# Performance work log

Measured on AMD Instinct MI355X. Metric: run time of the kernel, lower is better.

## Reference

```python
import jax, jax.numpy as jnp
import numpy as np

N, M, D, K = 32768, 1024, 512, 4096  # frames, motion_dim, latent_dim, codebook size
COMMITMENT_COST = 0.25
BN_EPS = 1e-5


def setup_inputs() -> dict:
    key = jax.random.key(0)
    ks = jax.random.split(key, 4)
    return {
        "x": jax.random.normal(ks[0], (N, M), dtype=jnp.float32),
        "enc_w": jax.random.normal(ks[1], (D, M), dtype=jnp.float32) * (1.0 / np.sqrt(M)),
        "enc_b": jnp.zeros((D,), jnp.float32),
        "bn_gamma": jnp.ones((D,), jnp.float32),
        "bn_beta": jnp.zeros((D,), jnp.float32),
        "bn_mean": jnp.zeros((D,), jnp.float32),
        "bn_var": jnp.ones((D,), jnp.float32),
        # nn.Embedding init: uniform(-1/K, 1/K)
        "codebook": jax.random.uniform(ks[2], (K, D), dtype=jnp.float32, minval=-1.0 / K, maxval=1.0 / K),
        "dec_w": jax.random.normal(ks[3], (M, D), dtype=jnp.float32) * (1.0 / np.sqrt(D)),
        "dec_b": jnp.zeros((M,), jnp.float32),
    }


def reference(x, enc_w, enc_b, bn_gamma, bn_beta, bn_mean, bn_var, codebook, dec_w, dec_b):
    # Encoder linear: [N, M] -> [N, D]
    z = x @ enc_w.T + enc_b
    # BatchNorm1d (inference mode, running stats)
    z = (z - bn_mean) * jax.lax.rsqrt(bn_var + BN_EPS) * bn_gamma + bn_beta

    # VQ (VQ_Payam_EMA, eval): squared L2 distances via ||z||^2 + ||e||^2 - 2 z e^T
    # distances: [N, K]
    distances = (
        jnp.sum(z * z, axis=1, keepdims=True)
        + jnp.sum(codebook * codebook, axis=1)
        - 2.0 * (z @ codebook.T)
    )
    idx = jnp.argmin(distances, axis=1)                    # [N]
    encodings = jax.nn.one_hot(idx, K, dtype=z.dtype)      # [N, K] one-hot scatter
    quantized = codebook[idx]                              # gather == encodings @ codebook

    # commitment loss (EMA variant: only e_latent_loss, quantized detached)
    e_latent_loss = jnp.mean((jax.lax.stop_gradient(quantized) - z) ** 2)
    loss = COMMITMENT_COST * e_latent_loss

    # straight-through estimator
    quantized_st = z + jax.lax.stop_gradient(quantized - z)

    avg_probs = jnp.mean(encodings, axis=0)                # [K]
    perplexity = jnp.exp(-jnp.sum(avg_probs * jnp.log(avg_probs + 1e-10)))

    # Decoder linear: [N, D] -> [N, M]
    out = quantized_st @ dec_w.T + dec_b
    return out, loss, perplexity, encodings
```

## Files before the change

### kernel.cpp

```cpp
#include <hip/hip_runtime.h>
#include <math.h>
#include <float.h>

#define N_FR 32768
#define M_DIM 1024
#define D_DIM 512
#define K_CB 4096

static const long long OUT_ELEMS = (long long)N_FR * M_DIM;
static const long long LOSS_OFF  = OUT_ELEMS;
static const long long ENC_OFF   = OUT_ELEMS + 2;
static const long long Z_OFF   = ENC_OFF + 2;
static const long long DC_OFF  = Z_OFF  + (long long)N_FR * D_DIM;
static const long long XH_OFF  = DC_OFF + (long long)K_CB * M_DIM;
static const long long XL_OFF  = XH_OFF + (long long)N_FR * M_DIM / 2;
static const long long WH_OFF  = XL_OFF + (long long)N_FR * M_DIM / 2;
static const long long WL_OFF  = WH_OFF + (long long)D_DIM * M_DIM / 2;
static const long long CH_OFF  = WL_OFF + (long long)D_DIM * M_DIM / 2;
static const long long CL_OFF  = CH_OFF + (long long)K_CB * D_DIM / 2;
static const long long ZH_OFF  = CL_OFF + (long long)K_CB * D_DIM / 2;
static const long long ZL_OFF  = ZH_OFF + (long long)N_FR * D_DIM / 2;
static const long long PV_OFF  = ZL_OFF + (long long)N_FR * D_DIM / 2;
static const long long PI_OFF  = PV_OFF + 4LL * N_FR;
static const long long DWH_OFF = PI_OFF + 4LL * N_FR;
static const long long DWL_OFF = DWH_OFF + (long long)M_DIM * D_DIM / 2;
static const long long SNP_OFF = DWL_OFF + (long long)M_DIM * D_DIM / 2;
static const long long LP_OFF  = SNP_OFF + 16LL * N_FR;

typedef __attribute__((ext_vector_type(8))) short bf16x8;
typedef __attribute__((ext_vector_type(8))) unsigned short u16x8;
typedef __attribute__((ext_vector_type(4))) float f32x4;

__device__ __forceinline__ unsigned short f2bf(float f) {
    unsigned u = __float_as_uint(f);
    return (unsigned short)((u + 0x7fffu + ((u >> 16) & 1u)) >> 16);
}
__device__ __forceinline__ float bf2f(unsigned short h) {
    return __uint_as_float(((unsigned)h) << 16);
}
__device__ __forceinline__ void gl_lds16(const unsigned short* g, unsigned short* l) {
    __builtin_amdgcn_global_load_lds(
        (const __attribute__((address_space(1))) unsigned int*)g,
        (__attribute__((address_space(3))) unsigned int*)l,
        16, 0, 0);
}

__device__ __forceinline__ void conv_body(const float* in, unsigned short* hi,
                                          unsigned short* lo, int C, int KC, int w)
{
    int lane = threadIdx.x & 63;
    int bn = w / KC, ck = w % KC;
    int r = bn * 16 + (lane & 15);
    int c = ck * 32 + (lane >> 4) * 8;
    const float4* p = (const float4*)&in[(size_t)r * C + c];
    float4 v0 = p[0], v1 = p[1];
    float f[8] = {v0.x, v0.y, v0.z, v0.w, v1.x, v1.y, v1.z, v1.w};
    u16x8 hv, lv;
    #pragma unroll
    for (int j = 0; j < 8; ++j) {
        unsigned short h = f2bf(f[j]);
        hv[j] = h;
        lv[j] = f2bf(f[j] - bf2f(h));
    }
    size_t o = (size_t)w * 512 + lane * 8;
    *(u16x8*)&hi[o] = hv;
    *(u16x8*)&lo[o] = lv;
}

__global__ __launch_bounds__(256)
void conv_all(const float* __restrict__ x,  const float* __restrict__ ew,
              const float* __restrict__ cb, const float* __restrict__ dw,
              unsigned short* __restrict__ xh,  unsigned short* __restrict__ xl,
              unsigned short* __restrict__ wh,  unsigned short* __restrict__ wl,
              unsigned short* __restrict__ ch,  unsigned short* __restrict__ cl,
              unsigned short* __restrict__ dwh, unsigned short* __restrict__ dwl)
{
    int b = blockIdx.x;
    const float* in; unsigned short* hi; unsigned short* lo; int C; int w0;
    if (b < 16384)      { in = x;  hi = xh;  lo = xl;  C = 1024; w0 = b; }
    else if (b < 16640) { in = ew; hi = wh;  lo = wl;  C = 1024; w0 = b - 16384; }
    else if (b < 17664) { in = cb; hi = ch;  lo = cl;  C = 512;  w0 = b - 16640; }
    else                { in = dw; hi = dwh; lo = dwl; C = 512;  w0 = b - 17664; }
    int KC = C / 32;
    conv_body(in, hi, lo, C, KC, w0 * 4 + (threadIdx.x >> 6));
}

__global__ __launch_bounds__(256)
void conv_z(const float* __restrict__ z, unsigned short* __restrict__ zh,
            unsigned short* __restrict__ zl, float* __restrict__ snp)
{
    int w = blockIdx.x * 4 + (threadIdx.x >> 6);
    int lane = threadIdx.x & 63;
    int bn = w >> 4, ck = w & 15;
    int r = bn * 16 + (lane & 15);
    int c = ck * 32 + (lane >> 4) * 8;
    const float4* p = (const float4*)&z[(size_t)r * D_DIM + c];
    float4 v0 = p[0], v1 = p[1];
    float f[8] = {v0.x, v0.y, v0.z, v0.w, v1.x, v1.y, v1.z, v1.w};
    u16x8 hv, lv;
    float s = 0.f;
    #pragma unroll
    for (int j = 0; j < 8; ++j) {
        unsigned short h = f2bf(f[j]);
        hv[j] = h;
        lv[j] = f2bf(f[j] - bf2f(h));
        s = fmaf(f[j], f[j], s);
    }
    size_t o = (size_t)w * 512 + lane * 8;
    *(u16x8*)&zh[o] = hv;
    *(u16x8*)&zl[o] = lv;
    s += __shfl_xor(s, 16);
    s += __shfl_xor(s, 32);
    if ((lane >> 4) == 0) snp[(size_t)ck * N_FR + r] = s;
}

template<int EPI>
__global__ __launch_bounds__(256, 2)
void gemm_pack(const unsigned short* __restrict__ ah_, const unsigned short* __restrict__ al_,
               const unsigned short* __restrict__ bh_, const unsigned short* __restrict__ bl_,
               const float* __restrict__ bias, const float* __restrict__ gamma,
               const float* __restrict__ beta, const float* __restrict__ mean,
               const float* __restrict__ var, float* __restrict__ C,
               int nbi, int nkb, int NJ)
{
    __shared__ unsigned short lds[32768];
    const int tid = threadIdx.x, wid = tid >> 6, lane = tid & 63;
    const int wr = wid >> 1, wc = wid & 1;
    const int bi = blockIdx.x % nbi, bj = blockIdx.x / nbi;

    auto stage = [&](int ks, int bufsel) {
        unsigned short* dst = lds + bufsel * 16384;
        #pragma unroll
        for (int q = 0; q < 8; ++q) {
            int id = wid * 8 + q;
            int arr = id >> 3, rb = id & 7;
            const unsigned short* base = arr == 0 ? ah_ : arr == 1 ? al_ : arr == 2 ? bh_ : bl_;
            size_t b = (size_t)((arr < 2 ? bi : bj) * 8 + rb) * nkb + ks;
            gl_lds16(base + b * 512 + lane * 8, dst + id * 512);
        }
    };

    f32x4 acc[4][4];
    #pragma unroll
    for (int i = 0; i < 4; ++i)
        #pragma unroll
        for (int j = 0; j < 4; ++j) acc[i][j] = (f32x4){0.f, 0.f, 0.f, 0.f};

    stage(0, 0);
    __syncthreads();

    for (int ks = 0; ks < nkb; ++ks) {
        int cur = ks & 1;
        if (ks + 1 < nkb) stage(ks + 1, cur ^ 1);
        const unsigned short* L = lds + cur * 16384;
        bf16x8 ah[4], al[4], bh[4], bl[4];
        #pragma unroll
        for (int i = 0; i < 4; ++i) {
            ah[i] = *(const bf16x8*)(L + (4 * wr + i) * 512 + lane * 8);
            al[i] = *(const bf16x8*)(L + 4096 + (4 * wr + i) * 512 + lane * 8);
        }
        #pragma unroll
        for (int j = 0; j < 4; ++j) {
            bh[j] = *(const bf16x8*)(L + 8192  + (4 * wc + j) * 512 + lane * 8);
            bl[j] = *(const bf16x8*)(L + 12288 + (4 * wc + j) * 512 + lane * 8);
        }
        #pragma unroll
        for (int i = 0; i < 4; ++i)
            #pragma unroll
            for (int j = 0; j < 4; ++j) {
                acc[i][j] = __builtin_amdgcn_mfma_f32_16x16x32_bf16(ah[i], bh[j], acc[i][j], 0, 0, 0);
                acc[i][j] = __builtin_amdgcn_mfma_f32_16x16x32_bf16(ah[i], bl[j], acc[i][j], 0, 0, 0);
                acc[i][j] = __builtin_amdgcn_mfma_f32_16x16x32_bf16(al[i], bh[j], acc[i][j], 0, 0, 0);
            }
        __syncthreads();
    }
    #pragma unroll
    for (int j = 0; j < 4; ++j) {
        int col = bj * 128 + wc * 64 + j * 16 + (lane & 15);
        float bvv = bias[col];
        float g = 0.f, bt = 0.f, mn = 0.f, rs = 0.f;
        if (EPI == 0) {
            g  = gamma[col];
            bt = beta[col];
            mn = mean[col];
            rs = (float)(1.0 / sqrt((double)var[col] + 1e-5));
        }
        #pragma unroll
        for (int i = 0; i < 4; ++i)
            #pragma unroll
            for (int r = 0; r < 4; ++r) {
                int row = bi * 128 + wr * 64 + i * 16 + (lane >> 4) * 4 + r;
                float v = acc[i][j][r] + bvv;
                if (EPI == 0) v = (v - mn) * rs * g + bt;
                C[(size_t)row * NJ + col] = v;
            }
    }
}

__global__ __launch_bounds__(256, 2)
void argmin_mfma(const unsigned short* __restrict__ zh, const unsigned short* __restrict__ zl,
                 const unsigned short* __restrict__ ch,
                 const float* __restrict__ se,
                 float* __restrict__ pval, int* __restrict__ pidx)
{
    __shared__ unsigned short lds[32768];
    __shared__ float sv[128][2];
    __shared__ int   si[128][2];
    const int tid = threadIdx.x, wid = tid >> 6, lane = tid & 63;
    const int wr = wid >> 1, wc = wid & 1;
    const int row0 = (int)(blockIdx.x & 255) * 128;
    const int grp  = (int)(blockIdx.x >> 8);

    auto stage = [&](int t, int bufsel) {
        int cc = t >> 4, ks = t & 15;
        int code0 = grp * 1024 + cc * 256;
        unsigned short* dst = lds + bufsel * 16384;
        #pragma unroll
        for (int q = 0; q < 8; ++q) {
            int id = wid * 8 + q;
            const unsigned short* src;
            if (id < 16) {
                int a = id >> 3, rb = id & 7;
                src = (a ? zl : zh) + ((size_t)((row0 >> 4) + rb) * 16 + ks) * 512 + lane * 8;
            } else {
                int cb2 = id - 16;
                src = ch + ((size_t)((code0 >> 4) + cb2) * 16 + ks) * 512 + lane * 8;
            }
            gl_lds16(src, dst + id * 512);
        }
    };

    float bv[16];
    int   bi[16];
    #pragma unroll
    for (int s = 0; s < 16; ++s) { bv[s] = FLT_MAX; bi[s] = 0x7fffffff; }

    f32x4 acc[4][8];
    #pragma unroll
    for (int i = 0; i < 4; ++i)
        #pragma unroll
        for (int j = 0; j < 8; ++j) acc[i][j] = (f32x4){0.f, 0.f, 0.f, 0.f};

    stage(0, 0);
    __syncthreads();

    for (int t = 0; t < 64; ++t) {
        int cur = t & 1;
        if (t < 63) stage(t + 1, cur ^ 1);
        const unsigned short* L = lds + cur * 16384;
        bf16x8 ah[4], al[4];
        #pragma unroll
        for (int i = 0; i < 4; ++i) {
            ah[i] = *(const bf16x8*)(L + (wr * 4 + i) * 512 + lane * 8);
            al[i] = *(const bf16x8*)(L + 4096 + (wr * 4 + i) * 512 + lane * 8);
        }
        #pragma unroll
        for (int j = 0; j < 8; ++j) {
            bf16x8 bhj = *(const bf16x8*)(L + 8192 + (wc * 8 + j) * 512 + lane * 8);
            #pragma unroll
            for (int i = 0; i < 4; ++i) {
                acc[i][j] = __builtin_amdgcn_mfma_f32_16x16x32_bf16(ah[i], bhj, acc[i][j], 0, 0, 0);
                acc[i][j] = __builtin_amdgcn_mfma_f32_16x16x32_bf16(al[i], bhj, acc[i][j], 0, 0, 0);
            }
        }
        if ((t & 15) == 15) {
            int code0 = grp * 1024 + (t >> 4) * 256;
            #pragma unroll
            for (int j = 0; j < 8; ++j) {
                int code = code0 + wc * 128 + j * 16 + (lane & 15);
                float sev = se[code];
                #pragma unroll
                for (int i = 0; i < 4; ++i)
                    #pragma unroll
                    for (int r = 0; r < 4; ++r) {
                        float key = sev - 2.0f * acc[i][j][r];
                        int s = i * 4 + r;
                        if (key < bv[s]) { bv[s] = key; bi[s] = code; }
                        acc[i][j][r] = 0.f;
                    }
            }
        }
        __syncthreads();
    }

    #pragma unroll
    for (int s = 0; s < 16; ++s) {
        #pragma unroll
        for (int off = 1; off < 16; off <<= 1) {
            float ov = __shfl_xor(bv[s], off);
            int   oi = __shfl_xor(bi[s], off);
            if (ov < bv[s] || (ov == bv[s] && oi < bi[s])) { bv[s] = ov; bi[s] = oi; }
        }
    }
    if ((lane & 15) == 0) {
        #pragma unroll
        for (int i = 0; i < 4; ++i)
            #pragma unroll
            for (int r = 0; r < 4; ++r) {
                int row = wr * 64 + i * 16 + (lane >> 4) * 4 + r;
                sv[row][wc] = bv[i * 4 + r];
                si[row][wc] = bi[i * 4 + r];
            }
    }
    __syncthreads();
    if (tid < 128) {
        float v0 = sv[tid][0], v1 = sv[tid][1];
        int   i0 = si[tid][0], i1 = si[tid][1];
        float bvv = v0; int bii = i0;
        if (v1 < v0 || (v1 == v0 && i1 < i0)) { bvv = v1; bii = i1; }
        pval[(size_t)grp * N_FR + row0 + tid] = bvv;
        pidx[(size_t)grp * N_FR + row0 + tid] = bii;
    }
}

__global__ __launch_bounds__(256)
void merge_k(const float* __restrict__ pval, const int* __restrict__ pidx,
             const float* __restrict__ snp,
             int* __restrict__ fidx, int* __restrict__ counts,
             float* __restrict__ lpart)
{
    __shared__ float ls[4];
    int tid = threadIdx.x;
    int n = blockIdx.x * 256 + tid;
    float best = pval[n];
    int   bi   = pidx[n];
    #pragma unroll
    for (int c = 1; c < 4; ++c) {
        float v = pval[(long long)c * N_FR + n];
        int   i = pidx[(long long)c * N_FR + n];
        if (v < best) { best = v; bi = i; }
    }
    fidx[n] = bi;
    atomicAdd(&counts[bi], 1);
    float sn = 0.f;
    #pragma unroll
    for (int c = 0; c < 16; ++c) sn += snp[(long long)c * N_FR + n];
    float rl = sn + best;
    #pragma unroll
    for (int off = 32; off; off >>= 1) rl += __shfl_xor(rl, off);
    if ((tid & 63) == 0) ls[tid >> 6] = rl;
    __syncthreads();
    if (tid == 0) lpart[blockIdx.x] = ls[0] + ls[1] + ls[2] + ls[3];
}

__global__ __launch_bounds__(256)
void rownorm_k(const float* __restrict__ A, float* __restrict__ sn,
               int* __restrict__ counts)
{
    if (blockIdx.x < 16) counts[blockIdx.x * 256 + threadIdx.x] = 0;
    int row  = blockIdx.x * 4 + (threadIdx.x >> 6);
    int lane = threadIdx.x & 63;
    const float4* p = (const float4*)(A + (long long)row * D_DIM + lane * 8);
    float4 a = p[0], b = p[1];
    float s = a.x*a.x + a.y*a.y + a.z*a.z + a.w*a.w
            + b.x*b.x + b.y*b.y + b.z*b.z + b.w*b.w;
    #pragma unroll
    for (int off = 32; off; off >>= 1) s += __shfl_xor(s, off);
    if (lane == 0) sn[row] = s;
}

__global__ __launch_bounds__(256)
void gather_k(const float* __restrict__ DC, const int* __restrict__ fidx,
              float* __restrict__ outp)
{
    int n = blockIdx.x;
    int id = fidx[n];
    float4 v = ((const float4*)(DC + (long long)id * M_DIM))[threadIdx.x];
    ((float4*)(outp + (long long)n * M_DIM))[threadIdx.x] = v;
}

__global__ __launch_bounds__(256)
void enc_write(const int* __restrict__ fidx, float* __restrict__ enc)
{
    int n    = blockIdx.x * 4 + (threadIdx.x >> 6);
    int lane = threadIdx.x & 63;
    int idx  = fidx[n];
    f32x4* row = (f32x4*)(enc + (size_t)n * K_CB);
    #pragma unroll
    for (int c = 0; c < 16; ++c) {
        int p = c * 64 + lane;
        int b4 = p * 4;
        f32x4 v;
        v.x = (idx == b4 + 0) ? 1.0f : 0.0f;
        v.y = (idx == b4 + 1) ? 1.0f : 0.0f;
        v.z = (idx == b4 + 2) ? 1.0f : 0.0f;
        v.w = (idx == b4 + 3) ? 1.0f : 0.0f;
        __builtin_nontemporal_store(v, &row[p]);
    }
}

__global__ __launch_bounds__(256)
void fin_k(const int* __restrict__ counts, const float* __restrict__ lpart,
           float* __restrict__ scal)
{
    __shared__ double sh[4], lh[4];
    int tid = threadIdx.x;
    double s = 0.0;
    for (int k = tid; k < K_CB; k += 256) {
        double p = (double)counts[k] / (double)N_FR;
        s += p * log(p + 1e-10);
    }
    double l = (tid < 128) ? (double)lpart[tid] : 0.0;
    #pragma unroll
    for (int off = 32; off; off >>= 1) {
        s += __shfl_xor(s, off);
        l += __shfl_xor(l, off);
    }
    if ((tid & 63) == 0) { sh[tid >> 6] = s; lh[tid >> 6] = l; }
    __syncthreads();
    if (tid == 0) {
        double tot = sh[0] + sh[1] + sh[2] + sh[3];
        double L   = lh[0] + lh[1] + lh[2] + lh[3];
        scal[0] = (float)(0.25 * L / ((double)N_FR * (double)D_DIM));
        scal[1] = (float)exp(-tot);
    }
}

extern "C" void kernel_launch(void* const* d_in, const int* in_sizes, int n_in,
                              void* d_out, int out_size, void* d_ws, size_t ws_size,
                              hipStream_t stream)
{
    (void)in_sizes; (void)n_in; (void)out_size; (void)ws_size;
    const float* x        = (const float*)d_in[0];
    const float* enc_w    = (const float*)d_in[1];
    const float* enc_b    = (const float*)d_in[2];
    const float* bn_gamma = (const float*)d_in[3];
    const float* bn_beta  = (const float*)d_in[4];
    const float* bn_mean  = (const float*)d_in[5];
    const float* bn_var   = (const float*)d_in[6];
    const float* cb       = (const float*)d_in[7];
    const float* dec_w    = (const float*)d_in[8];
    const float* dec_b    = (const float*)d_in[9];

    float* outp = (float*)d_out;
    float* z    = outp + Z_OFF;
    float* dc   = outp + DC_OFF;
    unsigned short* xh  = (unsigned short*)(outp + XH_OFF);
    unsigned short* xl  = (unsigned short*)(outp + XL_OFF);
    unsigned short* whp = (unsigned short*)(outp + WH_OFF);
    unsigned short* wlp = (unsigned short*)(outp + WL_OFF);
    unsigned short* chp = (unsigned short*)(outp + CH_OFF);
    unsigned short* clp = (unsigned short*)(outp + CL_OFF);
    unsigned short* zhp = (unsigned short*)(outp + ZH_OFF);
    unsigned short* zlp = (unsigned short*)(outp + ZL_OFF);
    float* pval = outp + PV_OFF;
    int*   pidx = (int*)(outp + PI_OFF);
    unsigned short* dwh = (unsigned short*)(outp + DWH_OFF);
    unsigned short* dwl = (unsigned short*)(outp + DWL_OFF);
    float* snp   = outp + SNP_OFF;
    float* lpart = outp + LP_OFF;

    char*   wsb    = (char*)d_ws;
    int*    fidx   = (int*)wsb;
    int*    counts = (int*)(wsb + 131072);
    float*  se     = (float*)(wsb + 147456);

    conv_all<<<dim3(17920), 256, 0, stream>>>(x, enc_w, cb, dec_w,
        xh, xl, whp, wlp, chp, clp, dwh, dwl);
    rownorm_k<<<dim3(K_CB / 4), 256, 0, stream>>>(cb, se, counts);

    gemm_pack<0><<<dim3(1024), 256, 0, stream>>>(xh, xl, whp, wlp,
        enc_b, bn_gamma, bn_beta, bn_mean, bn_var, z, 256, 32, D_DIM);
    conv_z<<<dim3(8192), 256, 0, stream>>>(z, zhp, zlp, snp);

    gemm_pack<1><<<dim3(256), 256, 0, stream>>>(chp, clp, dwh, dwl,
        dec_b, nullptr, nullptr, nullptr, nullptr, dc, 32, 16, M_DIM);

    argmin_mfma<<<dim3(1024), 256, 0, stream>>>(zhp, zlp, chp, se, pval, pidx);
    merge_k<<<dim3(N_FR / 256), 256, 0, stream>>>(pval, pidx, snp, fidx, counts, lpart);

    gather_k<<<dim3(N_FR), 256, 0, stream>>>(dc, fidx, outp);
    fin_k<<<dim3(1), 256, 0, stream>>>(counts, lpart, outp + LOSS_OFF);

    enc_write<<<dim3(N_FR / 4), 256, 0, stream>>>(fidx, outp + ENC_OFF);
}
```

Measured before the change: 648.3 us.

## Switch GEMMs and argmin to 32x32x16 MFMA with repacked 32-row bf16 tiles

Repacks the hi/lo bf16 operand tiles into 32-row by 16-column blocks and replaces the 16x16x32 MFMA calls with 32x32x16 MFMA in the encoder, decoder and distance GEMMs. Larger MFMA tiles mean fewer LDS fragment loads per flop and fewer instructions issued. The argmin epilogue now reduces across lanes at every 256-code chunk and keeps running minima in shared memory instead of per-thread registers. This adds shuffle and LDS work per chunk, and the per-row norm partials double to 32 slices.

```diff
diff --git a/kernel.cpp b/kernel.cpp
--- a/kernel.cpp
+++ b/kernel.cpp
@@ -25,11 +25,12 @@
 static const long long DWH_OFF = PI_OFF + 4LL * N_FR;
 static const long long DWL_OFF = DWH_OFF + (long long)M_DIM * D_DIM / 2;
 static const long long SNP_OFF = DWL_OFF + (long long)M_DIM * D_DIM / 2;
-static const long long LP_OFF  = SNP_OFF + 16LL * N_FR;
-
-typedef __attribute__((ext_vector_type(8))) short bf16x8;
-typedef __attribute__((ext_vector_type(8))) unsigned short u16x8;
-typedef __attribute__((ext_vector_type(4))) float f32x4;
+static const long long LP_OFF  = SNP_OFF + 32LL * N_FR;
+
+typedef __attribute__((ext_vector_type(8)))  short bf16x8;
+typedef __attribute__((ext_vector_type(8)))  unsigned short u16x8;
+typedef __attribute__((ext_vector_type(4)))  float f32x4;
+typedef __attribute__((ext_vector_type(16))) float f32x16;
 
 __device__ __forceinline__ unsigned short f2bf(float f) {
     unsigned u = __float_as_uint(f);
@@ -44,14 +45,18 @@
         (__attribute__((address_space(3))) unsigned int*)l,
         16, 0, 0);
 }
+__device__ __forceinline__ f32x16 zero16() {
+    f32x16 z = {0.f,0.f,0.f,0.f,0.f,0.f,0.f,0.f,0.f,0.f,0.f,0.f,0.f,0.f,0.f,0.f};
+    return z;
+}
 
 __device__ __forceinline__ void conv_body(const float* in, unsigned short* hi,
-                                          unsigned short* lo, int C, int KC, int w)
+                                          unsigned short* lo, int C, int KC16, int w)
 {
     int lane = threadIdx.x & 63;
-    int bn = w / KC, ck = w % KC;
-    int r = bn * 16 + (lane & 15);
-    int c = ck * 32 + (lane >> 4) * 8;
+    int bn = w / KC16, ck = w % KC16;
+    int r = bn * 32 + (lane & 31);
+    int c = ck * 16 + (lane >> 5) * 8;
     const float4* p = (const float4*)&in[(size_t)r * C + c];
     float4 v0 = p[0], v1 = p[1];
     float f[8] = {v0.x, v0.y, v0.z, v0.w, v1.x, v1.y, v1.z, v1.w};
@@ -81,8 +86,8 @@
     else if (b < 16640) { in = ew; hi = wh;  lo = wl;  C = 1024; w0 = b - 16384; }
     else if (b < 17664) { in = cb; hi = ch;  lo = cl;  C = 512;  w0 = b - 16640; }
     else                { in = dw; hi = dwh; lo = dwl; C = 512;  w0 = b - 17664; }
-    int KC = C / 32;
-    conv_body(in, hi, lo, C, KC, w0 * 4 + (threadIdx.x >> 6));
+    int KC16 = C / 16;
+    conv_body(in, hi, lo, C, KC16, w0 * 4 + (threadIdx.x >> 6));
 }
 
 __global__ __launch_bounds__(256)
@@ -91,9 +96,9 @@
 {
     int w = blockIdx.x * 4 + (threadIdx.x >> 6);
     int lane = threadIdx.x & 63;
-    int bn = w >> 4, ck = w & 15;
-    int r = bn * 16 + (lane & 15);
-    int c = ck * 32 + (lane >> 4) * 8;
+    int bn = w >> 5, ck = w & 31;
+    int r = bn * 32 + (lane & 31);
+    int c = ck * 16 + (lane >> 5) * 8;
     const float4* p = (const float4*)&z[(size_t)r * D_DIM + c];
     float4 v0 = p[0], v1 = p[1];
     float f[8] = {v0.x, v0.y, v0.z, v0.w, v1.x, v1.y, v1.z, v1.w};
@@ -109,9 +114,8 @@
     size_t o = (size_t)w * 512 + lane * 8;
     *(u16x8*)&zh[o] = hv;
     *(u16x8*)&zl[o] = lv;
-    s += __shfl_xor(s, 16);
     s += __shfl_xor(s, 32);
-    if ((lane >> 4) == 0) snp[(size_t)ck * N_FR + r] = s;
+    if (lane < 32) snp[(size_t)ck * N_FR + r] = s;
 }
 
 template<int EPI>
@@ -121,7 +125,7 @@
                const float* __restrict__ bias, const float* __restrict__ gamma,
                const float* __restrict__ beta, const float* __restrict__ mean,
                const float* __restrict__ var, float* __restrict__ C,
-               int nbi, int nkb, int NJ)
+               int nbi, int nsteps, int nkb16, int NJ)
 {
     __shared__ unsigned short lds[32768];
     const int tid = threadIdx.x, wid = tid >> 6, lane = tid & 63;
@@ -133,50 +137,57 @@
         #pragma unroll
         for (int q = 0; q < 8; ++q) {
             int id = wid * 8 + q;
-            int arr = id >> 3, rb = id & 7;
+            int arr = id >> 3, idx = id & 7, rb = idx >> 1, kb = idx & 1;
             const unsigned short* base = arr == 0 ? ah_ : arr == 1 ? al_ : arr == 2 ? bh_ : bl_;
-            size_t b = (size_t)((arr < 2 ? bi : bj) * 8 + rb) * nkb + ks;
+            int bsel = (arr < 2) ? bi : bj;
+            size_t b = (size_t)(bsel * 4 + rb) * nkb16 + ks * 2 + kb;
             gl_lds16(base + b * 512 + lane * 8, dst + id * 512);
         }
     };
 
-    f32x4 acc[4][4];
-    #pragma unroll
-    for (int i = 0; i < 4; ++i)
-        #pragma unroll
-        for (int j = 0; j < 4; ++j) acc[i][j] = (f32x4){0.f, 0.f, 0.f, 0.f};
+    f32x16 acc[2][2];
+    #pragma unroll
+    for (int i = 0; i < 2; ++i)
+        #pragma unroll
+        for (int j = 0; j < 2; ++j) acc[i][j] = zero16();
 
     stage(0, 0);
     __syncthreads();
 
-    for (int ks = 0; ks < nkb; ++ks) {
+    for (int ks = 0; ks < nsteps; ++ks) {
         int cur = ks & 1;
-        if (ks + 1 < nkb) stage(ks + 1, cur ^ 1);
+        if (ks + 1 < nsteps) stage(ks + 1, cur ^ 1);
         const unsigned short* L = lds + cur * 16384;
-        bf16x8 ah[4], al[4], bh[4], bl[4];
-        #pragma unroll
-        for (int i = 0; i < 4; ++i) {
-            ah[i] = *(const bf16x8*)(L + (4 * wr + i) * 512 + lane * 8);
-            al[i] = *(const bf16x8*)(L + 4096 + (4 * wr + i) * 512 + lane * 8);
-        }
-        #pragma unroll
-        for (int j = 0; j < 4; ++j) {
-            bh[j] = *(const bf16x8*)(L + 8192  + (4 * wc + j) * 512 + lane * 8);
-            bl[j] = *(const bf16x8*)(L + 12288 + (4 * wc + j) * 512 + lane * 8);
-        }
-        #pragma unroll
-        for (int i = 0; i < 4; ++i)
-            #pragma unroll
-            for (int j = 0; j < 4; ++j) {
-                acc[i][j] = __builtin_amdgcn_mfma_f32_16x16x32_bf16(ah[i], bh[j], acc[i][j], 0, 0, 0);
-                acc[i][j] = __builtin_amdgcn_mfma_f32_16x16x32_bf16(ah[i], bl[j], acc[i][j], 0, 0, 0);
-                acc[i][j] = __builtin_amdgcn_mfma_f32_16x16x32_bf16(al[i], bh[j], acc[i][j], 0, 0, 0);
-            }
+        bf16x8 ah[2][2], al[2][2];
+        #pragma unroll
+        for (int i = 0; i < 2; ++i)
+            #pragma unroll
+            for (int kb = 0; kb < 2; ++kb) {
+                int blk = (wr * 2 + i) * 2 + kb;
+                ah[i][kb] = *(const bf16x8*)(L + blk * 512 + lane * 8);
+                al[i][kb] = *(const bf16x8*)(L + 4096 + blk * 512 + lane * 8);
+            }
+        #pragma unroll
+        for (int j = 0; j < 2; ++j) {
+            #pragma unroll
+            for (int kb = 0; kb < 2; ++kb) {
+                int blk = (wc * 2 + j) * 2 + kb;
+                bf16x8 bhj = *(const bf16x8*)(L + 8192  + blk * 512 + lane * 8);
+                bf16x8 blj = *(const bf16x8*)(L + 12288 + blk * 512 + lane * 8);
+                #pragma unroll
+                for (int i = 0; i < 2; ++i) {
+                    acc[i][j] = __builtin_amdgcn_mfma_f32_32x32x16_bf16(ah[i][kb], bhj, acc[i][j], 0, 0, 0);
+                    acc[i][j] = __builtin_amdgcn_mfma_f32_32x32x16_bf16(ah[i][kb], blj, acc[i][j], 0, 0, 0);
+                    acc[i][j] = __builtin_amdgcn_mfma_f32_32x32x16_bf16(al[i][kb], bhj, acc[i][j], 0, 0, 0);
+                }
+            }
+        }
         __syncthreads();
     }
-    #pragma unroll
-    for (int j = 0; j < 4; ++j) {
-        int col = bj * 128 + wc * 64 + j * 16 + (lane & 15);
+
+    #pragma unroll
+    for (int j = 0; j < 2; ++j) {
+        int col = bj * 128 + wc * 64 + j * 32 + (lane & 31);
         float bvv = bias[col];
         float g = 0.f, bt = 0.f, mn = 0.f, rs = 0.f;
         if (EPI == 0) {
@@ -186,11 +197,11 @@
             rs = (float)(1.0 / sqrt((double)var[col] + 1e-5));
         }
         #pragma unroll
-        for (int i = 0; i < 4; ++i)
-            #pragma unroll
-            for (int r = 0; r < 4; ++r) {
-                int row = bi * 128 + wr * 64 + i * 16 + (lane >> 4) * 4 + r;
-                float v = acc[i][j][r] + bvv;
+        for (int i = 0; i < 2; ++i)
+            #pragma unroll
+            for (int reg = 0; reg < 16; ++reg) {
+                int row = bi * 128 + wr * 64 + i * 32 + (reg & 3) + 8 * (reg >> 2) + 4 * (lane >> 5);
+                float v = acc[i][j][reg] + bvv;
                 if (EPI == 0) v = (v - mn) * rs * g + bt;
                 C[(size_t)row * NJ + col] = v;
             }
@@ -220,26 +231,25 @@
             int id = wid * 8 + q;
             const unsigned short* src;
             if (id < 16) {
-                int a = id >> 3, rb = id & 7;
-                src = (a ? zl : zh) + ((size_t)((row0 >> 4) + rb) * 16 + ks) * 512 + lane * 8;
+                int a = id >> 3, idx = id & 7, rb = idx >> 1, kb = idx & 1;
+                size_t b = (size_t)((row0 >> 5) + rb) * 32 + ks * 2 + kb;
+                src = (a ? zl : zh) + b * 512 + lane * 8;
             } else {
-                int cb2 = id - 16;
-                src = ch + ((size_t)((code0 >> 4) + cb2) * 16 + ks) * 512 + lane * 8;
+                int idx = id - 16, cb2 = idx >> 1, kb = idx & 1;
+                size_t b = (size_t)((code0 >> 5) + cb2) * 32 + ks * 2 + kb;
+                src = ch + b * 512 + lane * 8;
             }
             gl_lds16(src, dst + id * 512);
         }
     };
 
-    float bv[16];
-    int   bi[16];
-    #pragma unroll
-    for (int s = 0; s < 16; ++s) { bv[s] = FLT_MAX; bi[s] = 0x7fffffff; }
-
-    f32x4 acc[4][8];
-    #pragma unroll
-    for (int i = 0; i < 4; ++i)
-        #pragma unroll
-        for (int j = 0; j < 8; ++j) acc[i][j] = (f32x4){0.f, 0.f, 0.f, 0.f};
+    if (tid < 256) { sv[tid >> 1][tid & 1] = FLT_MAX; si[tid >> 1][tid & 1] = 0x7fffffff; }
+
+    f32x16 acc[2][4];
+    #pragma unroll
+    for (int i = 0; i < 2; ++i)
+        #pragma unroll
+        for (int j = 0; j < 4; ++j) acc[i][j] = zero16();
 
     stage(0, 0);
     __syncthreads();
@@ -248,61 +258,69 @@
         int cur = t & 1;
         if (t < 63) stage(t + 1, cur ^ 1);
         const unsigned short* L = lds + cur * 16384;
-        bf16x8 ah[4], al[4];
-        #pragma unroll
-        for (int i = 0; i < 4; ++i) {
-            ah[i] = *(const bf16x8*)(L + (wr * 4 + i) * 512 + lane * 8);
-            al[i] = *(const bf16x8*)(L + 4096 + (wr * 4 + i) * 512 + lane * 8);
-        }
-        #pragma unroll
-        for (int j = 0; j < 8; ++j) {
-            bf16x8 bhj = *(const bf16x8*)(L + 8192 + (wc * 8 + j) * 512 + lane * 8);
-            #pragma unroll
-            for (int i = 0; i < 4; ++i) {
-                acc[i][j] = __builtin_amdgcn_mfma_f32_16x16x32_bf16(ah[i], bhj, acc[i][j], 0, 0, 0);
-                acc[i][j] = __builtin_amdgcn_mfma_f32_16x16x32_bf16(al[i], bhj, acc[i][j], 0, 0, 0);
+        bf16x8 ah[2][2], al[2][2];
+        #pragma unroll
+        for (int i = 0; i < 2; ++i)
+            #pragma unroll
+            for (int kb = 0; kb < 2; ++kb) {
+                int blk = (wr * 2 + i) * 2 + kb;
+                ah[i][kb] = *(const bf16x8*)(L + blk * 512 + lane * 8);
+                al[i][kb] = *(const bf16x8*)(L + 4096 + blk * 512 + lane * 8);
+            }
+        #pragma unroll
+        for (int j = 0; j < 4; ++j) {
+            #pragma unroll
+            for (int kb = 0; kb < 2; ++kb) {
+                int blk = (wc * 4 + j) * 2 + kb;
+                bf16x8 bhj = *(const bf16x8*)(L + 8192 + blk * 512 + lane * 8);
+                #pragma unroll
+                for (int i = 0; i < 2; ++i) {
+                    acc[i][j] = __builtin_amdgcn_mfma_f32_32x32x16_bf16(ah[i][kb], bhj, acc[i][j], 0, 0, 0);
+                    acc[i][j] = __builtin_amdgcn_mfma_f32_32x32x16_bf16(al[i][kb], bhj, acc[i][j], 0, 0, 0);
+                }
             }
         }
         if ((t & 15) == 15) {
-            int code0 = grp * 1024 + (t >> 4) * 256;
-            #pragma unroll
-            for (int j = 0; j < 8; ++j) {
-                int code = code0 + wc * 128 + j * 16 + (lane & 15);
-                float sev = se[code];
+            int code0g = grp * 1024 + (t >> 4) * 256;
+            float sev[4]; int codev[4];
+            #pragma unroll
+            for (int j = 0; j < 4; ++j) {
+                codev[j] = code0g + wc * 128 + j * 32 + (lane & 31);
+                sev[j] = se[codev[j]];
+            }
+            #pragma unroll
+            for (int i = 0; i < 2; ++i) {
                 #pragma unroll
-                for (int i = 0; i < 4; ++i)
+                for (int reg = 0; reg < 16; ++reg) {
+                    float bk = sev[0] - 2.0f * acc[i][0][reg];
+                    int   bc = codev[0];
                     #pragma unroll
-                    for (int r = 0; r < 4; ++r) {
-                        float key = sev - 2.0f * acc[i][j][r];
-                        int s = i * 4 + r;
-                        if (key < bv[s]) { bv[s] = key; bi[s] = code; }
-                        acc[i][j][r] = 0.f;
+                    for (int j = 1; j < 4; ++j) {
+                        float key = sev[j] - 2.0f * acc[i][j][reg];
+                        if (key < bk) { bk = key; bc = codev[j]; }
                     }
-            }
+                    #pragma unroll
+                    for (int off = 1; off < 32; off <<= 1) {
+                        float ov = __shfl_xor(bk, off);
+                        int   oc = __shfl_xor(bc, off);
+                        if (ov < bk || (ov == bk && oc < bc)) { bk = ov; bc = oc; }
+                    }
+                    if ((lane & 31) == 0) {
+                        int row = wr * 64 + i * 32 + (reg & 3) + 8 * (reg >> 2) + 4 * (lane >> 5);
+                        if (bk < sv[row][wc] || (bk == sv[row][wc] && bc < si[row][wc])) {
+                            sv[row][wc] = bk; si[row][wc] = bc;
+                        }
+                    }
+                }
+            }
+            #pragma unroll
+            for (int i = 0; i < 2; ++i)
+                #pragma unroll
+                for (int j = 0; j < 4; ++j) acc[i][j] = zero16();
         }
         __syncthreads();
     }
 
-    #pragma unroll
-    for (int s = 0; s < 16; ++s) {
-        #pragma unroll
-        for (int off = 1; off < 16; off <<= 1) {
-            float ov = __shfl_xor(bv[s], off);
-            int   oi = __shfl_xor(bi[s], off);
-            if (ov < bv[s] || (ov == bv[s] && oi < bi[s])) { bv[s] = ov; bi[s] = oi; }
-        }
-    }
-    if ((lane & 15) == 0) {
-        #pragma unroll
-        for (int i = 0; i < 4; ++i)
-            #pragma unroll
-            for (int r = 0; r < 4; ++r) {
-                int row = wr * 64 + i * 16 + (lane >> 4) * 4 + r;
-                sv[row][wc] = bv[i * 4 + r];
-                si[row][wc] = bi[i * 4 + r];
-            }
-    }
-    __syncthreads();
     if (tid < 128) {
         float v0 = sv[tid][0], v1 = sv[tid][1];
         int   i0 = si[tid][0], i1 = si[tid][1];
@@ -334,7 +352,7 @@
     atomicAdd(&counts[bi], 1);
     float sn = 0.f;
     #pragma unroll
-    for (int c = 0; c < 16; ++c) sn += snp[(long long)c * N_FR + n];
+    for (int c = 0; c < 32; ++c) sn += snp[(long long)c * N_FR + n];
     float rl = sn + best;
     #pragma unroll
     for (int off = 32; off; off >>= 1) rl += __shfl_xor(rl, off);
@@ -460,11 +478,11 @@
     rownorm_k<<<dim3(K_CB / 4), 256, 0, stream>>>(cb, se, counts);
 
     gemm_pack<0><<<dim3(1024), 256, 0, stream>>>(xh, xl, whp, wlp,
-        enc_b, bn_gamma, bn_beta, bn_mean, bn_var, z, 256, 32, D_DIM);
+        enc_b, bn_gamma, bn_beta, bn_mean, bn_var, z, 256, 32, 64, D_DIM);
     conv_z<<<dim3(8192), 256, 0, stream>>>(z, zhp, zlp, snp);
 
     gemm_pack<1><<<dim3(256), 256, 0, stream>>>(chp, clp, dwh, dwl,
-        dec_b, nullptr, nullptr, nullptr, nullptr, dc, 32, 16, M_DIM);
+        dec_b, nullptr, nullptr, nullptr, nullptr, dc, 32, 16, 32, M_DIM);
 
     argmin_mfma<<<dim3(1024), 256, 0, stream>>>(zhp, zlp, chp, se, pval, pidx);
     merge_k<<<dim3(N_FR / 256), 256, 0, stream>>>(pval, pidx, snp, fidx, counts, lpart);
```

Result: slower. 795.4 us (+22.7%).
